# Performance work log

Hardware: AMD Instinct MI355X
Metric: run time of the kernel (lower is better)

Reference implementation:

```python
import jax, jax.numpy as jnp
import numpy as np
import math

HIDDEN = 1024
HEADS = 16
HEAD_DIM = HIDDEN // HEADS
B, S = 4, 2048


def setup_inputs() -> dict:
    key = jax.random.key(0)
    ks = jax.random.split(key, 10)
    x = jax.random.normal(ks[0], (B, S, HIDDEN), dtype=jnp.float32)
    time_intervals = jax.random.uniform(ks[1], (B, S, S), dtype=jnp.float32)
    mask = jax.random.randint(ks[2], (B, 1, S, S), 0, 2, dtype=jnp.int32)
    scale = 1.0 / math.sqrt(HIDDEN)
    Wq = jax.random.normal(ks[3], (HIDDEN, HIDDEN), dtype=jnp.float32) * scale
    bq = jnp.zeros((HIDDEN,), dtype=jnp.float32)
    Wk = jax.random.normal(ks[4], (HIDDEN, HIDDEN), dtype=jnp.float32) * scale
    bk = jnp.zeros((HIDDEN,), dtype=jnp.float32)
    Wv = jax.random.normal(ks[5], (HIDDEN, HIDDEN), dtype=jnp.float32) * scale
    bv = jnp.zeros((HIDDEN,), dtype=jnp.float32)
    alpha = jnp.asarray(0.1, dtype=jnp.float32)
    return {"x": x, "time_intervals": time_intervals, "mask": mask,
            "Wq": Wq, "bq": bq, "Wk": Wk, "bk": bk, "Wv": Wv, "bv": bv,
            "alpha": alpha}


def reference(x, time_intervals, mask, Wq, bq, Wk, bk, Wv, bv, alpha):
    b, s, _ = x.shape
    # projections -> [b, heads, s, head_dim]
    def proj(W, bias):
        y = x @ W + bias
        return y.reshape(b, s, HEADS, HEAD_DIM).transpose(0, 2, 1, 3)
    Q = proj(Wq, bq)
    K = proj(Wk, bk)
    V = proj(Wv, bv)
    scores = jnp.einsum('bhqd,bhkd->bhqk', Q, K) / math.sqrt(HEAD_DIM)
    # additive time-decay bias, broadcast over heads
    scores = scores + (-jnp.abs(alpha)) * time_intervals[:, None, :, :]
    scores = jnp.where(mask == 0, jnp.float32(-1e9), scores)
    attn = jax.nn.softmax(scores, axis=-1)
    out = jnp.einsum('bhqk,bhkd->bhqd', attn, V)
    return out.transpose(0, 2, 1, 3).reshape(b, s, HIDDEN)
```

## Files before the change

kernel.cpp:

```cpp
#include <hip/hip_runtime.h>
#include <hip/hip_bf16.h>
#include <hip/hip_fp16.h>

#define BATCH 4
#define SEQ   2048
#define HID   1024
#define HEADS 16
#define HDIM  64
#define MROWS (BATCH * SEQ)
#define LOG2E 1.4426950408889634f
#define SCL   (LOG2E / 8.0f)

typedef _Float16 v8h __attribute__((ext_vector_type(8)));
typedef _Float16 v4h __attribute__((ext_vector_type(4)));
typedef _Float16 v2h __attribute__((ext_vector_type(2)));
typedef float    v4f __attribute__((ext_vector_type(4)));
typedef int      v4i __attribute__((ext_vector_type(4)));

#define MFMA16(a, b, c) __builtin_amdgcn_mfma_f32_16x16x32_f16((a), (b), (c), 0, 0, 0)

#if __has_builtin(__builtin_amdgcn_fdot2)
#define HAVE_FDOT2 1
#else
#define HAVE_FDOT2 0
#endif

__device__ inline int pk2(float a, float b) {
    return __builtin_bit_cast(int, __builtin_amdgcn_cvt_pkrtz(a, b));
}

__device__ __forceinline__ void async16(const void* g, void* l) {
    __builtin_amdgcn_global_load_lds(
        (const __attribute__((address_space(1))) unsigned int*)g,
        (__attribute__((address_space(3))) unsigned int*)l, 16, 0, 0);
}

#define SWZ(row, chunk) (((row) * 64) + ((((chunk) ^ ((row) & 7))) * 8))

__global__ __launch_bounds__(256) void cvt_x(const float* __restrict__ x,
                                             _Float16* __restrict__ xb) {
    int i = blockIdx.x * 256 + threadIdx.x;
    const float4* xp = (const float4*)x;
    float4 a = xp[2 * i];
    float4 b = xp[2 * i + 1];
    v4i o;
    o[0] = pk2(a.x, a.y); o[1] = pk2(a.z, a.w);
    o[2] = pk2(b.x, b.y); o[3] = pk2(b.z, b.w);
    ((v4i*)xb)[i] = o;
}

__global__ __launch_bounds__(256) void transw(const float* __restrict__ W,
                                              _Float16* __restrict__ Wt) {
    __shared__ float t[32][33];
    int bx = blockIdx.x * 32, by = blockIdx.y * 32;
    int tx = threadIdx.x, ty = threadIdx.y;
#pragma unroll
    for (int i = 0; i < 4; i++)
        t[ty + i * 8][tx] = W[(size_t)(by + ty + i * 8) * HID + bx + tx];
    __syncthreads();
#pragma unroll
    for (int i = 0; i < 4; i++)
        Wt[(size_t)(bx + ty + i * 8) * HID + by + tx] = (_Float16)t[tx][ty + i * 8];
}

__global__ __launch_bounds__(256) void mkbias(const float* __restrict__ tiv,
                                              const int* __restrict__ msk,
                                              const float* __restrict__ alphap,
                                              _Float16* __restrict__ biasT) {
    __shared__ _Float16 L[16 * 264];
    const int b = blockIdx.z, Q16 = blockIdx.y, kc0 = blockIdx.x * 256;
    const int tid = threadIdx.x;
    const float ca = -fabsf(alphap[0]) * LOG2E;
    const int prow = tid >> 6;
    const int pcol = (tid & 63) * 4;
#pragma unroll
    for (int pi = 0; pi < 4; pi++) {
        int r = pi * 4 + prow;
        size_t g = ((size_t)b * SEQ + Q16 * 16 + r) * SEQ + kc0 + pcol;
        float4 tv = *(const float4*)(tiv + g);
        int4   mv = *(const int4*)(msk + g);
        float f0 = mv.x ? ca * tv.x : -57344.0f;
        float f1 = mv.y ? ca * tv.y : -57344.0f;
        float f2 = mv.z ? ca * tv.z : -57344.0f;
        float f3 = mv.w ? ca * tv.w : -57344.0f;
        int2 o; o.x = pk2(f0, f1); o.y = pk2(f2, f3);
        *(int2*)&L[r * 264 + pcol] = o;
    }
    __syncthreads();
    const int lane = tid & 63, tq = tid >> 6;
#pragma unroll
    for (int it = 0; it < 4; it++) {
        int K16i = it * 4 + tq;
        int kl = K16i * 16 + (lane >> 4) * 4;
        int qr = lane & 15;
        int2 v = *(const int2*)&L[qr * 264 + kl];
        size_t o = ((((size_t)b * 128 + (kc0 >> 4) + K16i) * 128 + Q16) * 64 + lane) * 4;
        *(int2*)&biasT[o] = v;
    }
}

__global__ __launch_bounds__(256) void gemm_qkv(
    const _Float16* __restrict__ xb, const _Float16* __restrict__ wt,
    const float* __restrict__ bq, const float* __restrict__ bk,
    const float* __restrict__ bv,
    _Float16* __restrict__ Qb, _Float16* __restrict__ Kb, _Float16* __restrict__ Vtb) {
    const int mode = blockIdx.z;
    const _Float16* w = wt + (size_t)mode * HID * HID;
    __shared__ _Float16 As[128 * 64];
    __shared__ _Float16 Bs[128 * 64];
    const int tid = threadIdx.x;
    const int wv = tid >> 6, lane = tid & 63;
    const int quad = lane >> 4, l15 = lane & 15;
    const int wr = wv >> 1, wc = wv & 1;
    const int m0 = blockIdx.y * 128;
    const int n0 = blockIdx.x * 128;

    v4f acc[4][4];
#pragma unroll
    for (int i = 0; i < 4; i++)
#pragma unroll
        for (int j = 0; j < 4; j++) acc[i][j] = (v4f){0.f, 0.f, 0.f, 0.f};

    const int srow = lane >> 3;
    const int schk = lane & 7;
    const _Float16* Ag = xb + (size_t)m0 * HID;
    const _Float16* Bg = w + (size_t)n0 * HID;

    for (int k0 = 0; k0 < HID; k0 += 64) {
        __syncthreads();
#pragma unroll
        for (int i = 0; i < 4; i++) {
            int ra = wv * 32 + i * 8 + srow;
            int ca = schk ^ (ra & 7);
            async16(Ag + (size_t)ra * HID + k0 + ca * 8, &As[(wv * 32 + i * 8) * 64]);
            async16(Bg + (size_t)ra * HID + k0 + ca * 8, &Bs[(wv * 32 + i * 8) * 64]);
        }
        __syncthreads();
#pragma unroll
        for (int kc = 0; kc < 2; kc++) {
            v8h af[4], bf[4];
#pragma unroll
            for (int t = 0; t < 4; t++) {
                af[t] = *(const v8h*)&As[SWZ(wr * 64 + t * 16 + l15, kc * 4 + quad)];
                bf[t] = *(const v8h*)&Bs[SWZ(wc * 64 + t * 16 + l15, kc * 4 + quad)];
            }
#pragma unroll
            for (int tm = 0; tm < 4; tm++)
#pragma unroll
                for (int tn = 0; tn < 4; tn++)
                    acc[tm][tn] = MFMA16(af[tm], bf[tn], acc[tm][tn]);
        }
    }

    const float* pb = (mode == 0) ? bq : (mode == 1 ? bk : bv);
    const float oscl = (mode == 0) ? SCL : 1.0f;
#pragma unroll
    for (int tm = 0; tm < 4; tm++) {
#pragma unroll
        for (int tn = 0; tn < 4; tn++) {
            int n = n0 + wc * 64 + tn * 16 + l15;
            float bval = pb[n];
            int h = n >> 6, d = n & 63;
#pragma unroll
            for (int r = 0; r < 4; r++) {
                int m = m0 + wr * 64 + tm * 16 + quad * 4 + r;
                int b = m >> 11, s = m & 2047;
                _Float16 hv = (_Float16)((acc[tm][tn][r] + bval) * oscl);
                if (mode == 2) {
                    Vtb[(((size_t)(b * HEADS + h) * HDIM + d) * SEQ) + s] = hv;
                } else {
                    _Float16* dst = (mode == 0) ? Qb : Kb;
                    dst[((size_t)(b * HEADS + h) * SEQ + s) * HDIM + d] = hv;
                }
            }
        }
    }
}

__global__ __launch_bounds__(256, 4) void attn(
    const _Float16* __restrict__ Qb, const _Float16* __restrict__ Kb,
    const _Float16* __restrict__ Vtb, const _Float16* __restrict__ biasT,
    float* __restrict__ out) {
    const int bh = blockIdx.y;
    const int b = bh >> 4, h = bh & 15;
    const int qt = blockIdx.x;
    const int tid = threadIdx.x;
    const int wv = tid >> 6, lane = tid & 63;
    const int quad = lane >> 4, l15 = lane & 15;

    __shared__ _Float16 Ks[64 * 64];
    __shared__ _Float16 Vs[64 * 64];
    __shared__ _Float16 Ps[4][32 * 64];

    const int q0 = qt * 128 + wv * 32;
    const int Q16a = q0 >> 4;

    const _Float16* Qp = Qb + (size_t)(b * HEADS + h) * SEQ * HDIM;
    const _Float16* Kp = Kb + (size_t)(b * HEADS + h) * SEQ * HDIM;
    const _Float16* Vp = Vtb + (size_t)(b * HEADS + h) * HDIM * SEQ;
    const _Float16* Bbase = biasT + (size_t)b * 128 * 128 * 64 * 4;

    v8h qf[2][2];
#pragma unroll
    for (int tm = 0; tm < 2; tm++)
#pragma unroll
        for (int kc = 0; kc < 2; kc++)
            qf[tm][kc] = *(const v8h*)&Qp[(size_t)(q0 + tm * 16 + l15) * HDIM + kc * 32 + quad * 8];

    v4f oacc[2][4];
#pragma unroll
    for (int i = 0; i < 2; i++)
#pragma unroll
        for (int j = 0; j < 4; j++) oacc[i][j] = (v4f){0.f, 0.f, 0.f, 0.f};
    float lsum[2] = {0.f, 0.f};
#if HAVE_FDOT2
    const v2h one2 = {(_Float16)1.0f, (_Float16)1.0f};
#endif

    const int srow = lane >> 3, schk = lane & 7;

    for (int kt = 0; kt < SEQ / 64; kt++) {
        const int key0 = kt * 64;
        v4f sacc[4][2];
#pragma unroll
        for (int nt = 0; nt < 4; nt++)
#pragma unroll
            for (int tm = 0; tm < 2; tm++) {
                int2 bl = *(const int2*)&Bbase[((((size_t)(key0 >> 4) + nt) * 128 + Q16a + tm) * 64 + lane) * 4];
                v4h bv = __builtin_bit_cast(v4h, bl);
                sacc[nt][tm] = (v4f){(float)bv[0], (float)bv[1], (float)bv[2], (float)bv[3]};
            }

        __syncthreads();
#pragma unroll
        for (int i = 0; i < 2; i++) {
            int r = wv * 16 + i * 8 + srow;
            int c = schk ^ (r & 7);
            async16(Kp + (size_t)(key0 + r) * HDIM + c * 8, &Ks[(wv * 16 + i * 8) * 64]);
            async16(Vp + (size_t)r * SEQ + key0 + c * 8, &Vs[(wv * 16 + i * 8) * 64]);
        }
        __syncthreads();

#pragma unroll
        for (int kc = 0; kc < 2; kc++) {
            v8h kfr[4];
#pragma unroll
            for (int nt = 0; nt < 4; nt++)
                kfr[nt] = *(const v8h*)&Ks[SWZ(nt * 16 + l15, kc * 4 + quad)];
#pragma unroll
            for (int nt = 0; nt < 4; nt++)
#pragma unroll
                for (int tm = 0; tm < 2; tm++)
                    sacc[nt][tm] = MFMA16(kfr[nt], qf[tm][kc], sacc[nt][tm]);
        }

#pragma unroll
        for (int nt = 0; nt < 4; nt++)
#pragma unroll
            for (int tm = 0; tm < 2; tm++) {
                float p0 = __builtin_amdgcn_exp2f(sacc[nt][tm][0]);
                float p1 = __builtin_amdgcn_exp2f(sacc[nt][tm][1]);
                float p2 = __builtin_amdgcn_exp2f(sacc[nt][tm][2]);
                float p3 = __builtin_amdgcn_exp2f(sacc[nt][tm][3]);
                int2 pkv;
                pkv.x = pk2(p0, p1);
                pkv.y = pk2(p2, p3);
#if HAVE_FDOT2
                lsum[tm] = __builtin_amdgcn_fdot2(__builtin_bit_cast(v2h, pkv.x), one2, lsum[tm], false);
                lsum[tm] = __builtin_amdgcn_fdot2(__builtin_bit_cast(v2h, pkv.y), one2, lsum[tm], false);
#else
                lsum[tm] += (p0 + p1) + (p2 + p3);
#endif
                int q = tm * 16 + l15;
                int c16 = nt * 2 + (quad >> 1), half = quad & 1;
                *(int2*)&Ps[wv][q * 64 + ((c16 ^ (q & 7)) * 8) + half * 4] = pkv;
            }

#pragma unroll
        for (int kc = 0; kc < 2; kc++) {
            v8h pf[2], vfr[4];
#pragma unroll
            for (int tm = 0; tm < 2; tm++)
                pf[tm] = *(const v8h*)&Ps[wv][SWZ(tm * 16 + l15, kc * 4 + quad)];
#pragma unroll
            for (int nt = 0; nt < 4; nt++)
                vfr[nt] = *(const v8h*)&Vs[SWZ(nt * 16 + l15, kc * 4 + quad)];
#pragma unroll
            for (int tm = 0; tm < 2; tm++)
#pragma unroll
                for (int nt = 0; nt < 4; nt++)
                    oacc[tm][nt] = MFMA16(pf[tm], vfr[nt], oacc[tm][nt]);
        }
    }

#pragma unroll
    for (int tm = 0; tm < 2; tm++) {
        float lt = lsum[tm];
        lt += __shfl_xor(lt, 16);
        lt += __shfl_xor(lt, 32);
        float inv[4];
#pragma unroll
        for (int r = 0; r < 4; r++)
            inv[r] = 1.0f / __shfl(lt, quad * 4 + r);
#pragma unroll
        for (int nt = 0; nt < 4; nt++)
#pragma unroll
            for (int r = 0; r < 4; r++) {
                int q = q0 + tm * 16 + quad * 4 + r;
                int d = nt * 16 + l15;
                out[((size_t)b * SEQ + q) * HID + h * HDIM + d] = oacc[tm][nt][r] * inv[r];
            }
    }
}

extern "C" void kernel_launch(void* const* d_in, const int* in_sizes, int n_in,
                              void* d_out, int out_size, void* d_ws, size_t ws_size,
                              hipStream_t stream) {
    const float* x    = (const float*)d_in[0];
    const float* tiv  = (const float*)d_in[1];
    const int*   msk  = (const int*)d_in[2];
    const float* Wq   = (const float*)d_in[3];
    const float* bq   = (const float*)d_in[4];
    const float* Wk   = (const float*)d_in[5];
    const float* bk   = (const float*)d_in[6];
    const float* Wv   = (const float*)d_in[7];
    const float* bv   = (const float*)d_in[8];
    const float* alp  = (const float*)d_in[9];

    char* ws = (char*)d_ws;
    const size_t XB_OFF = 0;
    const size_t WT_OFF = XB_OFF + (size_t)MROWS * HID * 2;
    const size_t Q_OFF  = WT_OFF + (size_t)3 * HID * HID * 2;
    const size_t K_OFF  = Q_OFF + (size_t)MROWS * HID * 2;
    const size_t V_OFF  = K_OFF + (size_t)MROWS * HID * 2;
    const size_t B_OFF  = V_OFF + (size_t)MROWS * HID * 2;

    _Float16* xb   = (_Float16*)(ws + XB_OFF);
    _Float16* wt   = (_Float16*)(ws + WT_OFF);
    _Float16* Qb   = (_Float16*)(ws + Q_OFF);
    _Float16* Kb   = (_Float16*)(ws + K_OFF);
    _Float16* Vtb  = (_Float16*)(ws + V_OFF);
    _Float16* bias = (_Float16*)(ws + B_OFF);

    cvt_x<<<MROWS * HID / (256 * 8), 256, 0, stream>>>(x, xb);
    dim3 tb(32, 8);
    transw<<<dim3(32, 32), tb, 0, stream>>>(Wq, wt);
    transw<<<dim3(32, 32), tb, 0, stream>>>(Wk, wt + HID * HID);
    transw<<<dim3(32, 32), tb, 0, stream>>>(Wv, wt + 2 * HID * HID);
    mkbias<<<dim3(SEQ / 256, SEQ / 16, BATCH), 256, 0, stream>>>(tiv, msk, alp, bias);
    gemm_qkv<<<dim3(HID / 128, MROWS / 128, 3), 256, 0, stream>>>(
        xb, wt, bq, bk, bv, Qb, Kb, Vtb);
    attn<<<dim3(SEQ / 128, BATCH * HEADS), 256, 0, stream>>>(Qb, Kb, Vtb, bias,
                                                             (float*)d_out);
}
```

Before: 393.0 us.

## Keep softmax probabilities in registers for PV MFMA and merge weight transposes

```diff
diff --git a/kernel.cpp b/kernel.cpp
--- a/kernel.cpp
+++ b/kernel.cpp
@@ -18,12 +18,7 @@
 typedef int      v4i __attribute__((ext_vector_type(4)));
 
 #define MFMA16(a, b, c) __builtin_amdgcn_mfma_f32_16x16x32_f16((a), (b), (c), 0, 0, 0)
-
-#if __has_builtin(__builtin_amdgcn_fdot2)
-#define HAVE_FDOT2 1
-#else
-#define HAVE_FDOT2 0
-#endif
+#define MFMA16K16(a, b, c) __builtin_amdgcn_mfma_f32_16x16x16f16((a), (b), (c), 0, 0, 0)
 
 __device__ inline int pk2(float a, float b) {
     return __builtin_bit_cast(int, __builtin_amdgcn_cvt_pkrtz(a, b));
@@ -49,8 +44,12 @@
     ((v4i*)xb)[i] = o;
 }
 
-__global__ __launch_bounds__(256) void transw(const float* __restrict__ W,
+__global__ __launch_bounds__(256) void transw(const float* __restrict__ W0,
+                                              const float* __restrict__ W1,
+                                              const float* __restrict__ W2,
                                               _Float16* __restrict__ Wt) {
+    const float* W = (blockIdx.z == 0) ? W0 : (blockIdx.z == 1 ? W1 : W2);
+    _Float16* dst = Wt + (size_t)blockIdx.z * HID * HID;
     __shared__ float t[32][33];
     int bx = blockIdx.x * 32, by = blockIdx.y * 32;
     int tx = threadIdx.x, ty = threadIdx.y;
@@ -60,7 +59,7 @@
     __syncthreads();
 #pragma unroll
     for (int i = 0; i < 4; i++)
-        Wt[(size_t)(bx + ty + i * 8) * HID + by + tx] = (_Float16)t[tx][ty + i * 8];
+        dst[(size_t)(bx + ty + i * 8) * HID + by + tx] = (_Float16)t[tx][ty + i * 8];
 }
 
 __global__ __launch_bounds__(256) void mkbias(const float* __restrict__ tiv,
@@ -190,7 +189,6 @@
 
     __shared__ _Float16 Ks[64 * 64];
     __shared__ _Float16 Vs[64 * 64];
-    __shared__ _Float16 Ps[4][32 * 64];
 
     const int q0 = qt * 128 + wv * 32;
     const int Q16a = q0 >> 4;
@@ -213,9 +211,6 @@
 #pragma unroll
         for (int j = 0; j < 4; j++) oacc[i][j] = (v4f){0.f, 0.f, 0.f, 0.f};
     float lsum[2] = {0.f, 0.f};
-#if HAVE_FDOT2
-    const v2h one2 = {(_Float16)1.0f, (_Float16)1.0f};
-#endif
 
     const int srow = lane >> 3, schk = lane & 7;
 
@@ -254,6 +249,7 @@
                     sacc[nt][tm] = MFMA16(kfr[nt], qf[tm][kc], sacc[nt][tm]);
         }
 
+        int2 pfr[4][2];
 #pragma unroll
         for (int nt = 0; nt < 4; nt++)
 #pragma unroll
@@ -265,31 +261,26 @@
                 int2 pkv;
                 pkv.x = pk2(p0, p1);
                 pkv.y = pk2(p2, p3);
-#if HAVE_FDOT2
-                lsum[tm] = __builtin_amdgcn_fdot2(__builtin_bit_cast(v2h, pkv.x), one2, lsum[tm], false);
-                lsum[tm] = __builtin_amdgcn_fdot2(__builtin_bit_cast(v2h, pkv.y), one2, lsum[tm], false);
-#else
                 lsum[tm] += (p0 + p1) + (p2 + p3);
-#endif
-                int q = tm * 16 + l15;
-                int c16 = nt * 2 + (quad >> 1), half = quad & 1;
-                *(int2*)&Ps[wv][q * 64 + ((c16 ^ (q & 7)) * 8) + half * 4] = pkv;
-            }
-
-#pragma unroll
-        for (int kc = 0; kc < 2; kc++) {
-            v8h pf[2], vfr[4];
-#pragma unroll
-            for (int tm = 0; tm < 2; tm++)
-                pf[tm] = *(const v8h*)&Ps[wv][SWZ(tm * 16 + l15, kc * 4 + quad)];
-#pragma unroll
-            for (int nt = 0; nt < 4; nt++)
-                vfr[nt] = *(const v8h*)&Vs[SWZ(nt * 16 + l15, kc * 4 + quad)];
-#pragma unroll
-            for (int tm = 0; tm < 2; tm++)
+                pfr[nt][tm] = pkv;
+            }
+
+#pragma unroll
+        for (int g = 0; g < 4; g++) {
+            v4h vfr[4];
+#pragma unroll
+            for (int nt = 0; nt < 4; nt++) {
+                int row = nt * 16 + l15;
+                int cc = g * 2 + (quad >> 1);
+                vfr[nt] = *(const v4h*)&Vs[row * 64 + ((cc ^ (row & 7)) * 8) + (quad & 1) * 4];
+            }
+#pragma unroll
+            for (int tm = 0; tm < 2; tm++) {
+                v4h pa = __builtin_bit_cast(v4h, pfr[g][tm]);
 #pragma unroll
                 for (int nt = 0; nt < 4; nt++)
-                    oacc[tm][nt] = MFMA16(pf[tm], vfr[nt], oacc[tm][nt]);
+                    oacc[tm][nt] = MFMA16K16(pa, vfr[nt], oacc[tm][nt]);
+            }
         }
     }
 
@@ -344,9 +335,7 @@
 
     cvt_x<<<MROWS * HID / (256 * 8), 256, 0, stream>>>(x, xb);
     dim3 tb(32, 8);
-    transw<<<dim3(32, 32), tb, 0, stream>>>(Wq, wt);
-    transw<<<dim3(32, 32), tb, 0, stream>>>(Wk, wt + HID * HID);
-    transw<<<dim3(32, 32), tb, 0, stream>>>(Wv, wt + 2 * HID * HID);
+    transw<<<dim3(32, 32, 3), tb, 0, stream>>>(Wq, Wk, Wv, wt);
     mkbias<<<dim3(SEQ / 256, SEQ / 16, BATCH), 256, 0, stream>>>(tiv, msk, alp, bias);
     gemm_qkv<<<dim3(HID / 128, MROWS / 128, 3), 256, 0, stream>>>(
         xb, wt, bq, bk, bv, Qb, Kb, Vtb);
```

Result: no change. 392.7 us (-0.1%).
